# Kernel optimization log

Measured on AMD Instinct MI355X. Metric: run time of the kernel, lower is better.

## Reference

```python
import jax, jax.numpy as jnp
import numpy as np

B, S, D, H = 4, 2048, 512, 8
E = D // H  # d_head = 64

def setup_inputs() -> dict:
    key = jax.random.key(0)
    ks = jax.random.split(key, 10)
    s_in = (1.0 / np.sqrt(D))
    x  = jax.random.normal(ks[0], (B, S, D), dtype=jnp.float32)
    Wq = jax.random.normal(ks[1], (H, D, E), dtype=jnp.float32) * s_in
    bq = jax.random.normal(ks[2], (H, E), dtype=jnp.float32) * 0.01
    Wk = jax.random.normal(ks[3], (H, D, E), dtype=jnp.float32) * s_in
    bk = jax.random.normal(ks[4], (H, E), dtype=jnp.float32) * 0.01
    Wv = jax.random.normal(ks[5], (H, D, E), dtype=jnp.float32) * s_in
    bv = jax.random.normal(ks[6], (H, E), dtype=jnp.float32) * 0.01
    Wo = jax.random.normal(ks[7], (D, D), dtype=jnp.float32) * s_in
    bo = jax.random.normal(ks[8], (D,), dtype=jnp.float32) * 0.01
    return {"x": x, "Wq": Wq, "bq": bq, "Wk": Wk, "bk": bk,
            "Wv": Wv, "bv": bv, "Wo": Wo, "bo": bo}

def reference(x, Wq, bq, Wk, bk, Wv, bv, Wo, bo):
    B_, S_, D_ = x.shape
    # per-head projections (batched over head axis h)
    q = jnp.einsum('bsd,hde->bhse', x, Wq) + bq[None, :, None, :]
    k = jnp.einsum('bsd,hde->bhse', x, Wk) + bk[None, :, None, :]
    v = jnp.einsum('bsd,hde->bhse', x, Wv) + bv[None, :, None, :]
    # NOTE: original scales by d_model**-0.5 (full D), not d_head**-0.5
    scale = jnp.asarray(D_, x.dtype) ** -0.5
    scores = jnp.einsum('bhse,bhte->bhst', q, k) * scale  # [B,H,S,S]
    causal = jnp.tril(jnp.ones((S_, S_), dtype=bool))
    scores = jnp.where(causal[None, None], scores, -jnp.inf)
    attn = jax.nn.softmax(scores, axis=-1)
    out = jnp.einsum('bhst,bhte->bhse', attn, v)  # [B,H,S,E]
    # concat heads along feature dim (head-major), matching torch.cat
    out = out.transpose(0, 2, 1, 3).reshape(B_, S_, D_)
    return out @ Wo + bo  # final projection; dropout never applied in source
```

## Files before the change

kernel.cpp:

```cpp
#include <hip/hip_runtime.h>

typedef unsigned short u16;
typedef __bf16 bf16x8 __attribute__((ext_vector_type(8)));
typedef short s16x4 __attribute__((ext_vector_type(4)));
typedef short s16x8 __attribute__((ext_vector_type(8)));
typedef float f32x4 __attribute__((ext_vector_type(4)));

#define BB 4
#define SS 2048
#define DD 512
#define HH 8
#define EE 64
#define MM 8192
#define BHSE (BB*HH*SS*EE)

#define GLOBAL_AS __attribute__((address_space(1)))
#define LDS_AS    __attribute__((address_space(3)))

__device__ __forceinline__ float b2f(u16 u) {
    return __uint_as_float(((unsigned int)u) << 16);
}
__device__ __forceinline__ u16 f2b(float f) {
    unsigned int v = __float_as_uint(f);
    v += 0x7fffu + ((v >> 16) & 1u);
    return (u16)(v >> 16);
}
__device__ __forceinline__ float loadE(const void* p, size_t idx, int isbf16) {
    return isbf16 ? b2f(((const u16*)p)[idx]) : ((const float*)p)[idx];
}
__device__ __forceinline__ f32x4 mfma16x16x16_bf16(s16x4 a, s16x4 b, f32x4 c) {
    return __builtin_amdgcn_mfma_f32_16x16x16bf16_1k(a, b, c, 0, 0, 0);
}
__device__ __forceinline__ void load_lds16(const u16* g, u16* l) {
    __builtin_amdgcn_global_load_lds((GLOBAL_AS void*)g, (LDS_AS void*)l, 16, 0, 0);
}

__device__ __forceinline__ int detect_bf16(const u16* x) {
    int sane = 0;
    for (int i = 0; i < 128; ++i) {
        float a = fabsf(b2f(x[2 * i]));
        if (a == 0.f || (a > 1e-4f && a < 100.f)) ++sane;
    }
    return sane >= 96;
}

__global__ __launch_bounds__(256) void convert_x(
    const void* __restrict__ X, u16* __restrict__ Xb, int* __restrict__ flag)
{
    const int isbf16 = detect_bf16((const u16*)X);
    if (blockIdx.x == 0 && threadIdx.x == 0) *flag = isbf16;
    const size_t i0 = ((size_t)blockIdx.x * 256 + threadIdx.x) * 16;
    if (isbf16) {
        const uint4* src = (const uint4*)(((const u16*)X) + i0);
        uint4* dst = (uint4*)(Xb + i0);
        dst[0] = src[0];
        dst[1] = src[1];
    } else {
        const float* xf = ((const float*)X) + i0;
        float4 f0 = *(const float4*)xf;
        float4 f1 = *(const float4*)(xf + 4);
        float4 f2 = *(const float4*)(xf + 8);
        float4 f3 = *(const float4*)(xf + 12);
        u16 tmp[16] = { f2b(f0.x), f2b(f0.y), f2b(f0.z), f2b(f0.w),
                        f2b(f1.x), f2b(f1.y), f2b(f1.z), f2b(f1.w),
                        f2b(f2.x), f2b(f2.y), f2b(f2.z), f2b(f2.w),
                        f2b(f3.x), f2b(f3.y), f2b(f3.z), f2b(f3.w) };
        *(uint4*)(Xb + i0) = *(const uint4*)tmp;
        *(uint4*)(Xb + i0 + 8) = *(const uint4*)(tmp + 8);
    }
}

__global__ __launch_bounds__(256) void transpose_weights(
    const void* __restrict__ Wq, const void* __restrict__ Wk,
    const void* __restrict__ Wv, const void* __restrict__ Wo,
    u16* __restrict__ WT, u16* __restrict__ WoT, const int* __restrict__ flag)
{
    const int isbf16 = *flag;
    const int j = blockIdx.x;
    const int job = j >> 6;
    const int t = j & 63;
    const void* src; u16* dst; int src_ld, dst_ld;
    if (job < 3) {
        const void* W = (job == 0) ? Wq : ((job == 1) ? Wk : Wv);
        int h = t >> 3, kt = t & 7;
        size_t off = (size_t)h * DD * EE + (size_t)kt * 64 * EE;
        src = isbf16 ? (const void*)(((const u16*)W) + off)
                     : (const void*)(((const float*)W) + off);
        src_ld = EE;
        dst = WT + (size_t)job * 512 * 512 + (size_t)(h * 64) * 512 + kt * 64;
        dst_ld = 512;
    } else {
        int a = t >> 3, b = t & 7;
        size_t off = (size_t)(a * 64) * 512 + b * 64;
        src = isbf16 ? (const void*)(((const u16*)Wo) + off)
                     : (const void*)(((const float*)Wo) + off);
        src_ld = 512;
        dst = WoT + (size_t)(b * 64) * 512 + a * 64;
        dst_ld = 512;
    }
    __shared__ __align__(16) u16 Ts[64 * 72];
    const int tid = threadIdx.x;
#pragma unroll
    for (int it = 0; it < 2; ++it) {
        int idx = it * 256 + tid;
        int r = idx >> 3, c = (idx & 7) << 3;
#pragma unroll
        for (int k = 0; k < 8; ++k) {
            float v = loadE(src, (size_t)r * src_ld + c + k, isbf16);
            Ts[(c + k) * 72 + r] = f2b(v);
        }
    }
    __syncthreads();
#pragma unroll
    for (int it = 0; it < 2; ++it) {
        int idx = it * 256 + tid;
        int r = idx >> 3, c = (idx & 7) << 3;
        *(bf16x8*)(dst + (size_t)r * dst_ld + c) = *(const bf16x8*)&Ts[r * 72 + c];
    }
}

template<int MT, int NT>
__device__ __forceinline__ void mfma_step(const u16* As, const u16* Bs,
    int mh, int nh, int lq, int quad, f32x4 acc[MT][NT])
{
    const int sw = lq & 7;
#pragma unroll
    for (int kw = 0; kw < 2; ++kw) {
        const int G = kw * 4 + quad;
        const int col = ((G ^ sw) << 3);
        bf16x8 a[MT], b[NT];
#pragma unroll
        for (int mt = 0; mt < MT; ++mt)
            a[mt] = *(const bf16x8*)&As[(mh + mt * 16 + lq) * 64 + col];
#pragma unroll
        for (int nt = 0; nt < NT; ++nt)
            b[nt] = *(const bf16x8*)&Bs[(nh + nt * 16 + lq) * 64 + col];
#pragma unroll
        for (int mt = 0; mt < MT; ++mt)
#pragma unroll
            for (int nt = 0; nt < NT; ++nt)
                acc[mt][nt] = __builtin_amdgcn_mfma_f32_16x16x32_bf16(a[mt], b[nt], acc[mt][nt], 0, 0, 0);
    }
}

__global__ __launch_bounds__(256) void gemm_qkv(
    const u16* __restrict__ Xb, const u16* __restrict__ WT,
    const void* __restrict__ bq, const void* __restrict__ bk,
    const void* __restrict__ bv, u16* __restrict__ qkv,
    const int* __restrict__ flag)
{
    const float SCALE = 0.04419417382415922f;
    const int isbf16 = *flag;
    const int l = blockIdx.x;
    const int m0 = ((l & 7) * 8 + ((l >> 3) & 7)) * 128;
    const int n0 = (l >> 6) * 128;
    const int tid = threadIdx.x;
    const int wave = tid >> 6, lane = tid & 63;
    const int lq = lane & 15, quad = lane >> 4;
    const int mh = (wave & 1) * 64, nh = (wave >> 1) * 64;
    __shared__ __align__(16) u16 As[128 * 64];
    __shared__ __align__(16) u16 Bs[128 * 64];
    f32x4 acc[4][4] = {};

    const int swz = (lane & 7) ^ ((lane >> 3) & 7);
    const size_t lane_off = (size_t)(lane >> 3) * 512 + 8 * swz;

    for (int k0 = 0; k0 < 512; k0 += 64) {
        __syncthreads();
#pragma unroll
        for (int jj = 0; jj < 4; ++jj) {
            const int c = wave * 4 + jj;
            load_lds16(Xb + (size_t)(m0 + 8 * c) * 512 + k0 + lane_off, &As[c * 512]);
            load_lds16(WT + (size_t)(n0 + 8 * c) * 512 + k0 + lane_off, &Bs[c * 512]);
        }
        __syncthreads();
        mfma_step<4, 4>(As, Bs, mh, nh, lq, quad, acc);
    }

    const int proj = n0 >> 9;
    const void* bias = (proj == 0) ? bq : ((proj == 1) ? bk : bv);
#pragma unroll
    for (int mt = 0; mt < 4; ++mt) {
#pragma unroll
        for (int nt = 0; nt < 4; ++nt) {
#pragma unroll
            for (int r = 0; r < 4; ++r) {
                int m = m0 + mh + mt * 16 + quad * 4 + r;
                int n = n0 + nh + nt * 16 + lq;
                int nn = n & 511;
                float v = acc[mt][nt][r] + loadE(bias, nn, isbf16);
                if (proj == 0) v *= SCALE;
                int b_ = m >> 11, s = m & 2047, h = nn >> 6, e = nn & 63;
                qkv[(size_t)proj * BHSE + (((size_t)(b_ * HH + h) * SS + s) * EE + e)] = f2b(v);
            }
        }
    }
}

struct Stage { uint4 k0, k1, va, vb; };

__device__ __forceinline__ void stage_load(Stage& st, const u16* Kh, const u16* Vh,
                                           int t0, int tid) {
    int r = tid >> 3, c = (tid & 7) * 8;
    st.k0 = *(const uint4*)(Kh + (size_t)(t0 + r) * 64 + c);
    st.k1 = *(const uint4*)(Kh + (size_t)(t0 + r + 32) * 64 + c);
    int t2 = 2 * (tid & 31), e8 = (tid >> 5) * 8;
    st.va = *(const uint4*)(Vh + (size_t)(t0 + t2) * 64 + e8);
    st.vb = *(const uint4*)(Vh + (size_t)(t0 + t2 + 1) * 64 + e8);
}
__device__ __forceinline__ void stage_write(const Stage& st, u16* Ksb, u16* VTsb, int tid) {
    int r = tid >> 3, c = (tid & 7) * 8;
    *(uint4*)(Ksb + r * 72 + c) = st.k0;
    *(uint4*)(Ksb + (r + 32) * 72 + c) = st.k1;
    int t2 = 2 * (tid & 31), e8 = (tid >> 5) * 8;
    int g2 = ((t2 >> 2) & 3) * 16 + ((t2 >> 4) << 2) + (t2 & 3);
    const unsigned* pa = (const unsigned*)&st.va;
    const unsigned* pb = (const unsigned*)&st.vb;
#pragma unroll
    for (int k = 0; k < 4; ++k) {
        unsigned lo = __builtin_amdgcn_perm(pb[k], pa[k], 0x05040100u);
        unsigned hi = __builtin_amdgcn_perm(pb[k], pa[k], 0x07060302u);
        *(unsigned*)(VTsb + (e8 + 2 * k) * 72 + g2) = lo;
        *(unsigned*)(VTsb + (e8 + 2 * k + 1) * 72 + g2) = hi;
    }
}

__device__ __forceinline__ void attn_tile(const u16* Ksb, const u16* VTsb,
    bf16x8 qf0, bf16x8 qf1, int lq, int quad, int wave, bool diag,
    f32x4 Ot[4], float& lacc)
{
#pragma unroll
    for (int half = 0; half < 2; ++half) {
        s16x4 vf[4][2];
#pragma unroll
        for (int et = 0; et < 4; ++et) {
            const u16* Vp = VTsb + (et * 16 + lq) * 72 + quad * 16 + half * 8;
            s16x8 v = *(const s16x8*)Vp;
            vf[et][0] = __builtin_shufflevector(v, v, 0, 1, 2, 3);
            vf[et][1] = __builtin_shufflevector(v, v, 4, 5, 6, 7);
        }
#pragma unroll
        for (int tj = 0; tj < 2; ++tj) {
            const int tt = half * 2 + tj;
            const u16* Krow = Ksb + (tt * 16 + lq) * 72;
            bf16x8 k0 = *(const bf16x8*)(Krow + quad * 8);
            bf16x8 k1 = *(const bf16x8*)(Krow + 32 + quad * 8);
            f32x4 sc = {};
            sc = __builtin_amdgcn_mfma_f32_16x16x32_bf16(k0, qf0, sc, 0, 0, 0);
            sc = __builtin_amdgcn_mfma_f32_16x16x32_bf16(k1, qf1, sc, 0, 0, 0);
            unsigned pu[4];
#pragma unroll
            for (int r = 0; r < 4; ++r) {
                float p = __expf(sc[r]);
                if (diag) {
                    int tl = tt * 16 + quad * 4 + r;
                    int ql = 16 * wave + lq;
                    p = (tl <= ql) ? p : 0.f;
                }
                lacc += __uint_as_float(__float_as_uint(p) & 0xffff0000u);
                pu[r] = __float_as_uint(p);
            }
            union { unsigned u[2]; s16x4 s; } pf;
            pf.u[0] = __builtin_amdgcn_perm(pu[1], pu[0], 0x07060302u);
            pf.u[1] = __builtin_amdgcn_perm(pu[3], pu[2], 0x07060302u);
#pragma unroll
            for (int et = 0; et < 4; ++et)
                Ot[et] = mfma16x16x16_bf16(vf[et][tj], pf.s, Ot[et]);
        }
    }
}

__global__ __launch_bounds__(256) void attn_kernel(
    const u16* __restrict__ Qg, const u16* __restrict__ Kg,
    const u16* __restrict__ Vg, u16* __restrict__ Og)
{
    const int bh = blockIdx.x;
    const int qb = ((int)gridDim.y - 1 - (int)blockIdx.y) * 64;
    const int nt = qb >> 6;
    const int tid = threadIdx.x;
    const int wave = tid >> 6, lane = tid & 63;
    const int lq = lane & 15, quad = lane >> 4;
    const int b = bh >> 3, h = bh & 7;

    const size_t base = (size_t)bh * SS * EE;
    const u16* Kh = Kg + base;
    const u16* Vh = Vg + base;

    __shared__ __align__(16) u16 Ks[2][64 * 72];
    __shared__ __align__(16) u16 VTs[2][64 * 72];

    const int qrow = qb + 16 * wave + lq;
    const u16* Qp = Qg + base + (size_t)qrow * EE;
    bf16x8 qf0 = *(const bf16x8*)(Qp + quad * 8);
    bf16x8 qf1 = *(const bf16x8*)(Qp + 32 + quad * 8);

    f32x4 Ot[4] = {};
    float lacc = 0.f;

    Stage st;
    stage_load(st, Kh, Vh, 0, tid);
    stage_write(st, Ks[0], VTs[0], tid);
    for (int i = 0; i <= nt; ++i) {
        __syncthreads();
        const int cur = i & 1;
        const bool more = (i < nt);
        if (more) stage_load(st, Kh, Vh, (i + 1) * 64, tid);
        attn_tile(Ks[cur], VTs[cur], qf0, qf1, lq, quad, wave, i == nt, Ot, lacc);
        if (more) stage_write(st, Ks[cur ^ 1], VTs[cur ^ 1], tid);
    }

    lacc += __shfl_xor(lacc, 16);
    lacc += __shfl_xor(lacc, 32);
    const float inv = 1.f / lacc;

    u16* Op = Og + (((size_t)(b * SS + qrow)) * HH + h) * EE;
#pragma unroll
    for (int et = 0; et < 4; ++et) {
        u16 tmp[4];
#pragma unroll
        for (int r = 0; r < 4; ++r) tmp[r] = f2b(Ot[et][r] * inv);
        *(uint2*)(Op + et * 16 + quad * 4) = *(const uint2*)tmp;
    }
}

__global__ __launch_bounds__(256) void gemm_out(
    const u16* __restrict__ A, const u16* __restrict__ WoT,
    const void* __restrict__ bo, void* __restrict__ out,
    const int* __restrict__ flag)
{
    const int isbf16 = *flag;
    const int l = blockIdx.x;
    const int m0 = ((l & 7) * 8 + ((l >> 3) & 7)) * 128;
    const int n0 = (l >> 6) * 64;
    const int tid = threadIdx.x;
    const int wave = tid >> 6, lane = tid & 63;
    const int lq = lane & 15, quad = lane >> 4;
    const int mh = (wave & 1) * 64, nh = (wave >> 1) * 32;
    __shared__ __align__(16) u16 As[128 * 64];
    __shared__ __align__(16) u16 Bs[64 * 64];
    f32x4 acc[4][2] = {};

    const int swz = (lane & 7) ^ ((lane >> 3) & 7);
    const size_t lane_off = (size_t)(lane >> 3) * 512 + 8 * swz;

    for (int k0 = 0; k0 < 512; k0 += 64) {
        __syncthreads();
#pragma unroll
        for (int jj = 0; jj < 4; ++jj) {
            const int c = wave * 4 + jj;
            load_lds16(A + (size_t)(m0 + 8 * c) * 512 + k0 + lane_off, &As[c * 512]);
        }
#pragma unroll
        for (int jj = 0; jj < 2; ++jj) {
            const int c = wave * 2 + jj;
            load_lds16(WoT + (size_t)(n0 + 8 * c) * 512 + k0 + lane_off, &Bs[c * 512]);
        }
        __syncthreads();
        mfma_step<4, 2>(As, Bs, mh, nh, lq, quad, acc);
    }
#pragma unroll
    for (int mt = 0; mt < 4; ++mt) {
#pragma unroll
        for (int nt = 0; nt < 2; ++nt) {
#pragma unroll
            for (int r = 0; r < 4; ++r) {
                int m = m0 + mh + mt * 16 + quad * 4 + r;
                int n = n0 + nh + nt * 16 + lq;
                float v = acc[mt][nt][r] + loadE(bo, n, isbf16);
                if (isbf16) ((u16*)out)[(size_t)m * 512 + n] = f2b(v);
                else        ((float*)out)[(size_t)m * 512 + n] = v;
            }
        }
    }
}

extern "C" void kernel_launch(void* const* d_in, const int* in_sizes, int n_in,
                              void* d_out, int out_size, void* d_ws, size_t ws_size,
                              hipStream_t stream) {
    const void* x  = d_in[0];
    const void* Wq = d_in[1];
    const void* bq = d_in[2];
    const void* Wk = d_in[3];
    const void* bk = d_in[4];
    const void* Wv = d_in[5];
    const void* bv = d_in[6];
    const void* Wo = d_in[7];
    const void* bo = d_in[8];

    u16* WT   = (u16*)d_ws;
    u16* WoT  = WT + 3 * 512 * 512;
    u16* qkv  = WoT + 512 * 512;
    u16* attn = qkv + 3 * (size_t)BHSE;
    int* flag = (int*)(attn + (size_t)BHSE);
    u16* Xb   = (u16*)(flag + 8);

    convert_x<<<MM * DD / (256 * 16), 256, 0, stream>>>(x, Xb, flag);
    transpose_weights<<<256, 256, 0, stream>>>(Wq, Wk, Wv, Wo, WT, WoT, flag);
    gemm_qkv<<<(MM / 128) * (1536 / 128), 256, 0, stream>>>(Xb, WT, bq, bk, bv, qkv, flag);
    attn_kernel<<<dim3(BB * HH, SS / 64), 256, 0, stream>>>(qkv, qkv + BHSE, qkv + 2 * (size_t)BHSE, attn);
    gemm_out<<<(MM / 128) * (512 / 64), 256, 0, stream>>>(attn, WoT, bo, d_out, flag);
}
```

Before: 201.9 us.

## Use 128-row query blocks with 512 threads, MFMA row sums, wave-ballot dtype detect

The attention kernel now processes 128 query rows per block with 8 waves, so each K/V tile staged in LDS is shared by twice as many queries. K and V loading is split between the two thread halves. The softmax denominator is now computed by an extra MFMA against a ones vector instead of scalar adds and shuffles. The bf16 detection in convert_x is replaced by a wave ballot instead of a 128-iteration serial loop. The trade-offs are coarser causal work balance, since the upper waves idle on the last tile, and higher per-block resource use.

```diff
diff --git a/kernel.cpp b/kernel.cpp
--- a/kernel.cpp
+++ b/kernel.cpp
@@ -35,19 +35,20 @@
     __builtin_amdgcn_global_load_lds((GLOBAL_AS void*)g, (LDS_AS void*)l, 16, 0, 0);
 }
 
-__device__ __forceinline__ int detect_bf16(const u16* x) {
-    int sane = 0;
-    for (int i = 0; i < 128; ++i) {
-        float a = fabsf(b2f(x[2 * i]));
-        if (a == 0.f || (a > 1e-4f && a < 100.f)) ++sane;
-    }
-    return sane >= 96;
+__device__ __forceinline__ int detect_bf16_wave(const u16* x) {
+    const int lane = threadIdx.x & 63;
+    float a0 = fabsf(b2f(x[2 * lane]));
+    float a1 = fabsf(b2f(x[2 * (lane + 64)]));
+    int c0 = (a0 == 0.f) || (a0 > 1e-4f && a0 < 100.f);
+    int c1 = (a1 == 0.f) || (a1 > 1e-4f && a1 < 100.f);
+    int cnt = __popcll(__ballot(c0)) + __popcll(__ballot(c1));
+    return cnt >= 96;
 }
 
 __global__ __launch_bounds__(256) void convert_x(
     const void* __restrict__ X, u16* __restrict__ Xb, int* __restrict__ flag)
 {
-    const int isbf16 = detect_bf16((const u16*)X);
+    const int isbf16 = detect_bf16_wave((const u16*)X);
     if (blockIdx.x == 0 && threadIdx.x == 0) *flag = isbf16;
     const size_t i0 = ((size_t)blockIdx.x * 256 + threadIdx.x) * 16;
     if (isbf16) {
@@ -197,38 +198,47 @@
     }
 }
 
-struct Stage { uint4 k0, k1, va, vb; };
+struct Stage { uint4 a, b; };
 
 __device__ __forceinline__ void stage_load(Stage& st, const u16* Kh, const u16* Vh,
                                            int t0, int tid) {
-    int r = tid >> 3, c = (tid & 7) * 8;
-    st.k0 = *(const uint4*)(Kh + (size_t)(t0 + r) * 64 + c);
-    st.k1 = *(const uint4*)(Kh + (size_t)(t0 + r + 32) * 64 + c);
-    int t2 = 2 * (tid & 31), e8 = (tid >> 5) * 8;
-    st.va = *(const uint4*)(Vh + (size_t)(t0 + t2) * 64 + e8);
-    st.vb = *(const uint4*)(Vh + (size_t)(t0 + t2 + 1) * 64 + e8);
+    if (tid < 256) {
+        int r = tid >> 3, c = (tid & 7) * 8;
+        st.a = *(const uint4*)(Kh + (size_t)(t0 + r) * 64 + c);
+        st.b = *(const uint4*)(Kh + (size_t)(t0 + r + 32) * 64 + c);
+    } else {
+        int tv = tid - 256;
+        int t2 = 2 * (tv & 31), e8 = (tv >> 5) * 8;
+        st.a = *(const uint4*)(Vh + (size_t)(t0 + t2) * 64 + e8);
+        st.b = *(const uint4*)(Vh + (size_t)(t0 + t2 + 1) * 64 + e8);
+    }
 }
 __device__ __forceinline__ void stage_write(const Stage& st, u16* Ksb, u16* VTsb, int tid) {
-    int r = tid >> 3, c = (tid & 7) * 8;
-    *(uint4*)(Ksb + r * 72 + c) = st.k0;
-    *(uint4*)(Ksb + (r + 32) * 72 + c) = st.k1;
-    int t2 = 2 * (tid & 31), e8 = (tid >> 5) * 8;
-    int g2 = ((t2 >> 2) & 3) * 16 + ((t2 >> 4) << 2) + (t2 & 3);
-    const unsigned* pa = (const unsigned*)&st.va;
-    const unsigned* pb = (const unsigned*)&st.vb;
-#pragma unroll
-    for (int k = 0; k < 4; ++k) {
-        unsigned lo = __builtin_amdgcn_perm(pb[k], pa[k], 0x05040100u);
-        unsigned hi = __builtin_amdgcn_perm(pb[k], pa[k], 0x07060302u);
-        *(unsigned*)(VTsb + (e8 + 2 * k) * 72 + g2) = lo;
-        *(unsigned*)(VTsb + (e8 + 2 * k + 1) * 72 + g2) = hi;
+    if (tid < 256) {
+        int r = tid >> 3, c = (tid & 7) * 8;
+        *(uint4*)(Ksb + r * 72 + c) = st.a;
+        *(uint4*)(Ksb + (r + 32) * 72 + c) = st.b;
+    } else {
+        int tv = tid - 256;
+        int t2 = 2 * (tv & 31), e8 = (tv >> 5) * 8;
+        int g2 = ((t2 >> 2) & 3) * 16 + ((t2 >> 4) << 2) + (t2 & 3);
+        const unsigned* pa = (const unsigned*)&st.a;
+        const unsigned* pb = (const unsigned*)&st.b;
+#pragma unroll
+        for (int k = 0; k < 4; ++k) {
+            unsigned lo = __builtin_amdgcn_perm(pb[k], pa[k], 0x05040100u);
+            unsigned hi = __builtin_amdgcn_perm(pb[k], pa[k], 0x07060302u);
+            *(unsigned*)(VTsb + (e8 + 2 * k) * 72 + g2) = lo;
+            *(unsigned*)(VTsb + (e8 + 2 * k + 1) * 72 + g2) = hi;
+        }
     }
 }
 
 __device__ __forceinline__ void attn_tile(const u16* Ksb, const u16* VTsb,
-    bf16x8 qf0, bf16x8 qf1, int lq, int quad, int wave, bool diag,
-    f32x4 Ot[4], float& lacc)
-{
+    bf16x8 qf0, bf16x8 qf1, int lq, int quad, int ql64, bool diag,
+    f32x4 Ot[4], f32x4& lfrag)
+{
+    const s16x4 ones = { (short)0x3F80, (short)0x3F80, (short)0x3F80, (short)0x3F80 };
 #pragma unroll
     for (int half = 0; half < 2; ++half) {
         s16x4 vf[4][2];
@@ -254,15 +264,14 @@
                 float p = __expf(sc[r]);
                 if (diag) {
                     int tl = tt * 16 + quad * 4 + r;
-                    int ql = 16 * wave + lq;
-                    p = (tl <= ql) ? p : 0.f;
+                    p = (tl <= ql64) ? p : 0.f;
                 }
-                lacc += __uint_as_float(__float_as_uint(p) & 0xffff0000u);
                 pu[r] = __float_as_uint(p);
             }
             union { unsigned u[2]; s16x4 s; } pf;
             pf.u[0] = __builtin_amdgcn_perm(pu[1], pu[0], 0x07060302u);
             pf.u[1] = __builtin_amdgcn_perm(pu[3], pu[2], 0x07060302u);
+            lfrag = mfma16x16x16_bf16(ones, pf.s, lfrag);
 #pragma unroll
             for (int et = 0; et < 4; ++et)
                 Ot[et] = mfma16x16x16_bf16(vf[et][tj], pf.s, Ot[et]);
@@ -270,17 +279,20 @@
     }
 }
 
-__global__ __launch_bounds__(256) void attn_kernel(
+__global__ __launch_bounds__(512, 8) void attn_kernel(
     const u16* __restrict__ Qg, const u16* __restrict__ Kg,
     const u16* __restrict__ Vg, u16* __restrict__ Og)
 {
     const int bh = blockIdx.x;
-    const int qb = ((int)gridDim.y - 1 - (int)blockIdx.y) * 64;
-    const int nt = qb >> 6;
+    const int qb = ((int)gridDim.y - 1 - (int)blockIdx.y) * 128;
+    const int NT = (qb >> 6) + 2;
     const int tid = threadIdx.x;
     const int wave = tid >> 6, lane = tid & 63;
     const int lq = lane & 15, quad = lane >> 4;
     const int b = bh >> 3, h = bh & 7;
+    const int qh = wave >> 2;
+    const int ql64 = 16 * (wave & 3) + lq;
+    const int tdiag = (qb >> 6) + qh;
 
     const size_t base = (size_t)bh * SS * EE;
     const u16* Kh = Kg + base;
@@ -289,29 +301,28 @@
     __shared__ __align__(16) u16 Ks[2][64 * 72];
     __shared__ __align__(16) u16 VTs[2][64 * 72];
 
-    const int qrow = qb + 16 * wave + lq;
+    const int qrow = qb + qh * 64 + 16 * (wave & 3) + lq;
     const u16* Qp = Qg + base + (size_t)qrow * EE;
     bf16x8 qf0 = *(const bf16x8*)(Qp + quad * 8);
     bf16x8 qf1 = *(const bf16x8*)(Qp + 32 + quad * 8);
 
     f32x4 Ot[4] = {};
-    float lacc = 0.f;
+    f32x4 lfrag = {};
 
     Stage st;
     stage_load(st, Kh, Vh, 0, tid);
     stage_write(st, Ks[0], VTs[0], tid);
-    for (int i = 0; i <= nt; ++i) {
+    for (int i = 0; i < NT; ++i) {
         __syncthreads();
         const int cur = i & 1;
-        const bool more = (i < nt);
+        const bool more = (i + 1 < NT);
         if (more) stage_load(st, Kh, Vh, (i + 1) * 64, tid);
-        attn_tile(Ks[cur], VTs[cur], qf0, qf1, lq, quad, wave, i == nt, Ot, lacc);
+        if (i <= tdiag)
+            attn_tile(Ks[cur], VTs[cur], qf0, qf1, lq, quad, ql64, i == tdiag, Ot, lfrag);
         if (more) stage_write(st, Ks[cur ^ 1], VTs[cur ^ 1], tid);
     }
 
-    lacc += __shfl_xor(lacc, 16);
-    lacc += __shfl_xor(lacc, 32);
-    const float inv = 1.f / lacc;
+    const float inv = 1.f / lfrag[0];
 
     u16* Op = Og + (((size_t)(b * SS + qrow)) * HH + h) * EE;
 #pragma unroll
@@ -397,6 +408,6 @@
     convert_x<<<MM * DD / (256 * 16), 256, 0, stream>>>(x, Xb, flag);
     transpose_weights<<<256, 256, 0, stream>>>(Wq, Wk, Wv, Wo, WT, WoT, flag);
     gemm_qkv<<<(MM / 128) * (1536 / 128), 256, 0, stream>>>(Xb, WT, bq, bk, bv, qkv, flag);
-    attn_kernel<<<dim3(BB * HH, SS / 64), 256, 0, stream>>>(qkv, qkv + BHSE, qkv + 2 * (size_t)BHSE, attn);
+    attn_kernel<<<dim3(BB * HH, SS / 128), 512, 0, stream>>>(qkv, qkv + BHSE, qkv + 2 * (size_t)BHSE, attn);
     gemm_out<<<(MM / 128) * (512 / 64), 256, 0, stream>>>(attn, WoT, bo, d_out, flag);
 }
```

Measured after the change: 197.8 us. 1.02x faster.
